# Performance work log

Measured on AMD Instinct MI355X. Metric: run time of the kernel, lower is better.

## Reference

```python
import jax, jax.numpy as jnp
import numpy as np

E = 16          # num_local_experts
K = 4           # experts_per_token
H = 2048        # hidden_size
I = 2048        # intermediate_size
LIMIT = 7.0     # swiglu_limit
ALPHA = 1.702   # glu_alpha


def setup_inputs() -> dict:
    key = jax.random.key(0)
    ks = jax.random.split(key, 9)
    int8 = lambda k, shp: jax.random.randint(k, shp, -127, 128).astype(jnp.float32)
    return {
        "hidden_states": jax.random.normal(ks[0], (1024, H), dtype=jnp.float32),
        "router_logits": jax.random.normal(ks[1], (1024, E), dtype=jnp.float32),
        "gate_up_proj": int8(ks[2], (E, H, 2 * I)),                      # int8 values in f32
        "gate_up_proj_scale": jax.random.uniform(ks[3], (E, 2 * I), minval=0.5, maxval=1.5) * 0.002,
        "gate_up_proj_bias": jax.random.normal(ks[4], (E, 2 * I), dtype=jnp.float32) * 0.01,
        "gate_up_smooth_scale": jnp.ones((E, I), dtype=jnp.float32),
        "down_proj": int8(ks[5], (E, I, H)),
        "down_proj_scale": jax.random.uniform(ks[6], (E, H), minval=0.5, maxval=1.5) * 0.002,
        "down_proj_bias": jax.random.normal(ks[7], (E, H), dtype=jnp.float32) * 0.01,
    }


def _dyn_quant(x):
    # per-token symmetric int8 dynamic quant (npu_dynamic_quant)
    scale = jnp.maximum(jnp.max(jnp.abs(x), axis=-1, keepdims=True) / 127.0, 1e-8)
    q = jnp.clip(jnp.round(x / scale), -127.0, 127.0)
    return q, scale


def reference(hidden_states, router_logits, gate_up_proj, gate_up_proj_scale,
              gate_up_proj_bias, gate_up_smooth_scale, down_proj,
              down_proj_scale, down_proj_bias):
    T = hidden_states.shape[0]
    C = (2 * T * K) // E

    # --- gating (npu_moe_gating_top_k: softmax + top-k, then renormalize) ---
    probs = jax.nn.softmax(router_logits, axis=-1)
    topk_w, topk_i = jax.lax.top_k(probs, K)                 # [T,K]
    topk_w = topk_w / jnp.sum(topk_w, axis=-1, keepdims=True)

    # --- per-token dynamic quant ---
    x_q, x_scale = _dyn_quant(hidden_states)                 # [T,H], [T,1]

    # --- dispatch (npu_moe_init_routing_v2): token-major expansion, capacity buckets ---
    flat_e = topk_i.reshape(-1)                              # [T*K] expert id per row
    flat_w = topk_w.reshape(-1)                              # [T*K]
    src = jnp.arange(T * K) // K                             # [T*K] source token
    onehot = jax.nn.one_hot(flat_e, E, dtype=jnp.int32)      # [T*K,E]
    pos = jnp.sum(jnp.cumsum(onehot, axis=0) * onehot, axis=1) - 1  # position within expert
    valid = pos < C
    slot = flat_e * C + jnp.where(valid, pos, 0)             # unique for valid rows
    vf = valid.astype(x_q.dtype)[:, None]
    x_disp = jnp.zeros((E * C, H), x_q.dtype).at[slot].add(x_q[src] * vf)
    s_disp = jnp.zeros((E * C, 1), x_scale.dtype).at[slot].add(x_scale[src] * vf)
    x_disp = x_disp.reshape(E, C, H)
    s_disp = s_disp.reshape(E, C, 1)

    gu_i32 = jnp.einsum('ech,ehf->ecf', x_disp, gate_up_proj)          # [E,C,2I]
    y = gu_i32 * s_disp * gate_up_proj_scale[:, None, :] + gate_up_proj_bias[:, None, :]

    # --- gpt-oss swiglu (activate_left, clamp_limit, alpha=1.702, glu_bias=1.0) ---
    gate = jnp.minimum(y[..., :I], LIMIT)
    up = jnp.clip(y[..., I:], -LIMIT, LIMIT)
    act = gate * jax.nn.sigmoid(ALPHA * gate) * (up + 1.0)
    act = act * gate_up_smooth_scale[:, None, :]

    # --- requant + grouped GEMM 2 + dequant ---
    h_q, h_scale = _dyn_quant(act)                                     # [E,C,I], [E,C,1]
    z_i32 = jnp.einsum('eci,eih->ech', h_q, down_proj)                 # [E,C,H]
    z = z_i32 * h_scale * down_proj_scale[:, None, :] + down_proj_bias[:, None, :]

    # --- combine (npu_moe_finalize_routing): weighted scatter-add per source token ---
    gathered = z.reshape(E * C, H)[slot]                               # [T*K,H]
    out = jnp.zeros((T, H), z.dtype).at[src].add(flat_w[:, None] * vf * gathered)
    return out
```

## Files before the change

### kernel.cpp

```cpp
#include <hip/hip_runtime.h>
#include <stdint.h>
#include <stddef.h>

#define T_TOK 1024
#define NE    16
#define TOPK  4
#define HID   2048
#define INTER 2048
#define CAP   512
#define GLIMIT 7.0f
#define GALPHA 1.702f

#define BM  128
#define BK  64

typedef __attribute__((ext_vector_type(4))) int   iv4;

typedef const __attribute__((address_space(1))) unsigned gl_u32;
typedef __attribute__((address_space(3))) unsigned lds_u32;
__device__ __forceinline__ void gl_lds16(const void* g, void* l) {
    __builtin_amdgcn_global_load_lds((gl_u32*)g, (lds_u32*)l, 16, 0, 0);
}

__device__ __forceinline__ int pack4(float a, float b, float c, float d) {
    int qa = (int)a, qb = (int)b, qc = (int)c, qd = (int)d;
    return (qa & 255) | ((qb & 255) << 8) | ((qc & 255) << 16) | (qd << 24);
}

__global__ __launch_bounds__(256) void gating_kernel(
    const float* __restrict__ logits, int* __restrict__ topki, float* __restrict__ topkw)
{
    int t = blockIdx.x * 256 + threadIdx.x;
    if (t >= T_TOK) return;
    float l[NE];
#pragma unroll
    for (int e = 0; e < NE; e++) l[e] = logits[t * NE + e];
    unsigned used = 0;
    float val[TOPK]; int idx[TOPK];
#pragma unroll
    for (int k = 0; k < TOPK; k++) {
        float bv = -3.4e38f; int bi = 0;
#pragma unroll
        for (int e = 0; e < NE; e++) {
            bool ok = (((used >> e) & 1u) == 0u) && (l[e] > bv);
            bv = ok ? l[e] : bv;
            bi = ok ? e : bi;
        }
        used |= (1u << bi); idx[k] = bi; val[k] = bv;
    }
    float m = val[0];
    float s = 0.f, w[TOPK];
#pragma unroll
    for (int k = 0; k < TOPK; k++) { w[k] = expf(val[k] - m); s += w[k]; }
    float inv = 1.0f / s;
#pragma unroll
    for (int k = 0; k < TOPK; k++) { topki[t * TOPK + k] = idx[k]; topkw[t * TOPK + k] = w[k] * inv; }
}

__global__ __launch_bounds__(256) void quant_x_kernel(
    const float* __restrict__ x, char* __restrict__ xq, float* __restrict__ xs)
{
    int t = blockIdx.x;
    const float4* row = (const float4*)(x + (size_t)t * HID);
    __shared__ float red[256];
    float4 v0 = row[threadIdx.x];
    float4 v1 = row[threadIdx.x + 256];
    float amax = fmaxf(fmaxf(fabsf(v0.x), fabsf(v0.y)), fmaxf(fabsf(v0.z), fabsf(v0.w)));
    amax = fmaxf(amax, fmaxf(fmaxf(fabsf(v1.x), fabsf(v1.y)), fmaxf(fabsf(v1.z), fabsf(v1.w))));
    red[threadIdx.x] = amax; __syncthreads();
    for (int s = 128; s > 0; s >>= 1) {
        if (threadIdx.x < s) red[threadIdx.x] = fmaxf(red[threadIdx.x], red[threadIdx.x + s]);
        __syncthreads();
    }
    float scale = fmaxf(red[0] / 127.0f, 1e-8f);
    if (threadIdx.x == 0) xs[t] = scale;
    char4* orow = (char4*)(xq + (size_t)t * HID);
    {
        char4 c;
        c.x = (char)fminf(fmaxf(rintf(v0.x / scale), -127.f), 127.f);
        c.y = (char)fminf(fmaxf(rintf(v0.y / scale), -127.f), 127.f);
        c.z = (char)fminf(fmaxf(rintf(v0.z / scale), -127.f), 127.f);
        c.w = (char)fminf(fmaxf(rintf(v0.w / scale), -127.f), 127.f);
        orow[threadIdx.x] = c;
        c.x = (char)fminf(fmaxf(rintf(v1.x / scale), -127.f), 127.f);
        c.y = (char)fminf(fmaxf(rintf(v1.y / scale), -127.f), 127.f);
        c.z = (char)fminf(fmaxf(rintf(v1.z / scale), -127.f), 127.f);
        c.w = (char)fminf(fmaxf(rintf(v1.w / scale), -127.f), 127.f);
        orow[threadIdx.x + 256] = c;
    }
}

__global__ __launch_bounds__(1024) void routing_kernel(
    const int* __restrict__ topki, const float* __restrict__ topkw,
    int* __restrict__ row_src, float* __restrict__ row_w, int* __restrict__ counts)
{
    int wv = threadIdx.x >> 6;
    int lane = threadIdx.x & 63;
    int base = 0;
    for (int r0 = 0; r0 < T_TOK * TOPK; r0 += 64) {
        int r = r0 + lane;
        int e = topki[r];
        unsigned long long mask = __ballot(e == wv);
        int pre = __popcll(mask & ((1ULL << lane) - 1ULL));
        if (e == wv) {
            int pos = base + pre;
            if (pos < CAP) {
                row_src[wv * CAP + pos] = r >> 2;
                row_w[wv * CAP + pos] = topkw[r];
            }
        }
        base += __popcll(mask);
    }
    if (lane == 0) counts[wv] = (base < CAP) ? base : CAP;
}

__global__ __launch_bounds__(256) void gemm1_kernel(
    const char* __restrict__ xq, const float* __restrict__ xs,
    const int* __restrict__ row_src, const int* __restrict__ counts,
    const float* __restrict__ gup, const float* __restrict__ gus,
    const float* __restrict__ gub, const float* __restrict__ smo,
    float* __restrict__ act)
{
    int nt = blockIdx.x;
    int mt = blockIdx.y;
    int e  = blockIdx.z;
    int count = counts[e];
    int m0 = mt * BM;
    if (m0 >= count) return;

    __shared__ char sA[BM * BK];
    __shared__ char sB[128 * BK];

    int t = threadIdx.x;
    int lane = t & 63, w = t >> 6;
    int n16 = lane & 15, quad = lane >> 4;
    int swq = quad ^ ((n16 >> 1) & 3);

    const char* aSrc[2];
#pragma unroll
    for (int op = 0; op < 2; op++) {
        int c = op * 256 + t;
        int row = c >> 2, ks = c & 3;
        int ksg = ks ^ ((row >> 1) & 3);
        int gr = m0 + row;
        if (gr > count - 1) gr = count - 1;
        aSrc[op] = xq + (size_t)row_src[e * CAP + gr] * HID + ksg * 16;
    }

    int bc = t & 63;
    const float* bgate = gup + (size_t)e * HID * (2 * INTER) + nt * 64 + bc;
    const float* bup   = bgate + INTER;
    int sn = (bc >> 1) & 3;
    char* wpg = sB + bc * 64        + (w ^ sn) * 16;
    char* wpu = sB + (64 + bc) * 64 + (w ^ sn) * 16;

    iv4 acc[2][8];
#pragma unroll
    for (int i = 0; i < 2; i++)
#pragma unroll
        for (int j = 0; j < 8; j++) acc[i][j] = (iv4)0;

    float f[32];
#pragma unroll
    for (int i = 0; i < 16; i++) {
        f[i]      = bgate[(size_t)(w * 16 + i) * (2 * INTER)];
        f[16 + i] = bup  [(size_t)(w * 16 + i) * (2 * INTER)];
    }

    for (int kt = 0; kt < HID / BK; kt++) {
        __syncthreads();
        gl_lds16(aSrc[0] + kt * BK, sA + w * 1024);
        gl_lds16(aSrc[1] + kt * BK, sA + 4096 + w * 1024);
        {
            int d0[4], d1[4];
#pragma unroll
            for (int j = 0; j < 4; j++) {
                d0[j] = pack4(f[4 * j],      f[4 * j + 1],      f[4 * j + 2],      f[4 * j + 3]);
                d1[j] = pack4(f[16 + 4 * j], f[16 + 4 * j + 1], f[16 + 4 * j + 2], f[16 + 4 * j + 3]);
            }
            *(int4*)wpg = make_int4(d0[0], d0[1], d0[2], d0[3]);
            *(int4*)wpu = make_int4(d1[0], d1[1], d1[2], d1[3]);
        }
        __syncthreads();

        iv4 af[2], bf[8];
#pragma unroll
        for (int mf = 0; mf < 2; mf++)
            af[mf] = *(const iv4*)(sA + (w * 32 + mf * 16 + n16) * 64 + swq * 16);
#pragma unroll
        for (int nf = 0; nf < 8; nf++)
            bf[nf] = *(const iv4*)(sB + (nf * 16 + n16) * 64 + swq * 16);

        int kn = (kt + 1 < HID / BK) ? (kt + 1) : kt;
        size_t krow = (size_t)(kn * BK) * (2 * INTER);
#pragma unroll
        for (int i = 0; i < 16; i++) {
            f[i]      = bgate[krow + (size_t)(w * 16 + i) * (2 * INTER)];
            f[16 + i] = bup  [krow + (size_t)(w * 16 + i) * (2 * INTER)];
        }

#pragma unroll
        for (int mf = 0; mf < 2; mf++)
#pragma unroll
            for (int nf = 0; nf < 8; nf++)
                acc[mf][nf] = __builtin_amdgcn_mfma_i32_16x16x64_i8(af[mf], bf[nf], acc[mf][nf], 0, 0, 0);
    }

    const float* gsc = gus + (size_t)e * (2 * INTER);
    const float* gbi = gub + (size_t)e * (2 * INTER);
    const float* sms = smo + (size_t)e * INTER;
#pragma unroll
    for (int mf = 0; mf < 2; mf++) {
#pragma unroll
        for (int r = 0; r < 4; r++) {
            int gr = m0 + w * 32 + mf * 16 + quad * 4 + r;
            if (gr >= count) continue;
            float srow = xs[row_src[e * CAP + gr]];
            float* arow = act + (size_t)(e * CAP + gr) * INTER;
#pragma unroll
            for (int g = 0; g < 4; g++) {
                int col = nt * 64 + g * 16 + n16;
                float yg = (float)acc[mf][g][r]     * srow * gsc[col]         + gbi[col];
                float yu = (float)acc[mf][g + 4][r] * srow * gsc[INTER + col] + gbi[INTER + col];
                float gate = fminf(yg, GLIMIT);
                float up   = fminf(fmaxf(yu, -GLIMIT), GLIMIT);
                float sig  = 1.0f / (1.0f + expf(-GALPHA * gate));
                arow[col] = gate * sig * (up + 1.0f) * sms[col];
            }
        }
    }
}

__global__ __launch_bounds__(256) void requant_kernel(
    const float* __restrict__ act, const int* __restrict__ counts,
    char* __restrict__ hq, float* __restrict__ hs)
{
    int b = blockIdx.x;
    int e = b >> 9, c = b & (CAP - 1);
    if (c >= counts[e]) return;
    const float4* row = (const float4*)(act + (size_t)b * INTER);
    __shared__ float red[256];
    float4 v0 = row[threadIdx.x];
    float4 v1 = row[threadIdx.x + 256];
    float amax = fmaxf(fmaxf(fabsf(v0.x), fabsf(v0.y)), fmaxf(fabsf(v0.z), fabsf(v0.w)));
    amax = fmaxf(amax, fmaxf(fmaxf(fabsf(v1.x), fabsf(v1.y)), fmaxf(fabsf(v1.z), fabsf(v1.w))));
    red[threadIdx.x] = amax; __syncthreads();
    for (int s = 128; s > 0; s >>= 1) {
        if (threadIdx.x < s) red[threadIdx.x] = fmaxf(red[threadIdx.x], red[threadIdx.x + s]);
        __syncthreads();
    }
    float scale = fmaxf(red[0] / 127.0f, 1e-8f);
    if (threadIdx.x == 0) hs[b] = scale;
    char4* orow = (char4*)(hq + (size_t)b * INTER);
    {
        char4 cc;
        cc.x = (char)fminf(fmaxf(rintf(v0.x / scale), -127.f), 127.f);
        cc.y = (char)fminf(fmaxf(rintf(v0.y / scale), -127.f), 127.f);
        cc.z = (char)fminf(fmaxf(rintf(v0.z / scale), -127.f), 127.f);
        cc.w = (char)fminf(fmaxf(rintf(v0.w / scale), -127.f), 127.f);
        orow[threadIdx.x] = cc;
        cc.x = (char)fminf(fmaxf(rintf(v1.x / scale), -127.f), 127.f);
        cc.y = (char)fminf(fmaxf(rintf(v1.y / scale), -127.f), 127.f);
        cc.z = (char)fminf(fmaxf(rintf(v1.z / scale), -127.f), 127.f);
        cc.w = (char)fminf(fmaxf(rintf(v1.w / scale), -127.f), 127.f);
        orow[threadIdx.x + 256] = cc;
    }
}

__global__ __launch_bounds__(256) void gemm2_kernel(
    const char* __restrict__ hq, const float* __restrict__ hs,
    const int* __restrict__ row_src, const float* __restrict__ row_w,
    const int* __restrict__ counts, const float* __restrict__ dwn,
    const float* __restrict__ dsc, const float* __restrict__ dbi,
    float* __restrict__ out)
{
    int nt = blockIdx.x;
    int mt = blockIdx.y;
    int e  = blockIdx.z;
    int count = counts[e];
    int m0 = mt * BM;
    if (m0 >= count) return;

    __shared__ char sA[BM * BK];
    __shared__ char sB[128 * BK];

    int t = threadIdx.x;
    int lane = t & 63, w = t >> 6;
    int n16 = lane & 15, quad = lane >> 4;
    int swq = quad ^ ((n16 >> 1) & 3);

    const char* aSrc[2];
#pragma unroll
    for (int op = 0; op < 2; op++) {
        int c = op * 256 + t;
        int row = c >> 2, ks = c & 3;
        int ksg = ks ^ ((row >> 1) & 3);
        int gr = m0 + row;
        if (gr > count - 1) gr = count - 1;
        aSrc[op] = hq + (size_t)(e * CAP + gr) * INTER + ksg * 16;
    }

    int bc = t & 127;
    int half = t >> 7;
    const float* bsrc = dwn + (size_t)e * INTER * HID + nt * 128 + bc;
    int sn = (bc >> 1) & 3;
    char* wp0 = sB + bc * 64 + ((half * 2 + 0) ^ sn) * 16;
    char* wp1 = sB + bc * 64 + ((half * 2 + 1) ^ sn) * 16;

    iv4 acc[2][8];
#pragma unroll
    for (int i = 0; i < 2; i++)
#pragma unroll
        for (int j = 0; j < 8; j++) acc[i][j] = (iv4)0;

    float f[32];
#pragma unroll
    for (int i = 0; i < 32; i++)
        f[i] = bsrc[(size_t)(half * 32 + i) * HID];

    for (int kt = 0; kt < INTER / BK; kt++) {
        __syncthreads();
        gl_lds16(aSrc[0] + kt * BK, sA + w * 1024);
        gl_lds16(aSrc[1] + kt * BK, sA + 4096 + w * 1024);
        {
            int d[8];
#pragma unroll
            for (int j = 0; j < 8; j++)
                d[j] = pack4(f[4 * j], f[4 * j + 1], f[4 * j + 2], f[4 * j + 3]);
            *(int4*)wp0 = make_int4(d[0], d[1], d[2], d[3]);
            *(int4*)wp1 = make_int4(d[4], d[5], d[6], d[7]);
        }
        __syncthreads();

        iv4 af[2], bf[8];
#pragma unroll
        for (int mf = 0; mf < 2; mf++)
            af[mf] = *(const iv4*)(sA + (w * 32 + mf * 16 + n16) * 64 + swq * 16);
#pragma unroll
        for (int nf = 0; nf < 8; nf++)
            bf[nf] = *(const iv4*)(sB + (nf * 16 + n16) * 64 + swq * 16);

        int kn = (kt + 1 < INTER / BK) ? (kt + 1) : kt;
        size_t krow = (size_t)(kn * BK) * HID;
#pragma unroll
        for (int i = 0; i < 32; i++)
            f[i] = bsrc[krow + (size_t)(half * 32 + i) * HID];

#pragma unroll
        for (int mf = 0; mf < 2; mf++)
#pragma unroll
            for (int nf = 0; nf < 8; nf++)
                acc[mf][nf] = __builtin_amdgcn_mfma_i32_16x16x64_i8(af[mf], bf[nf], acc[mf][nf], 0, 0, 0);
    }

    const float* dscE = dsc + (size_t)e * HID;
    const float* dbiE = dbi + (size_t)e * HID;
#pragma unroll
    for (int mf = 0; mf < 2; mf++) {
#pragma unroll
        for (int r = 0; r < 4; r++) {
            int gr = m0 + w * 32 + mf * 16 + quad * 4 + r;
            if (gr >= count) continue;
            int ri = e * CAP + gr;
            float hsr = hs[ri];
            float wr  = row_w[ri];
            float* orow = out + (size_t)row_src[ri] * HID;
#pragma unroll
            for (int nf = 0; nf < 8; nf++) {
                int col = nt * 128 + nf * 16 + n16;
                float z = (float)acc[mf][nf][r] * hsr * dscE[col] + dbiE[col];
                atomicAdd(&orow[col], wr * z);
            }
        }
    }
}

extern "C" void kernel_launch(void* const* d_in, const int* in_sizes, int n_in,
                              void* d_out, int out_size, void* d_ws, size_t ws_size,
                              hipStream_t stream)
{
    (void)in_sizes; (void)n_in; (void)out_size; (void)ws_size;
    const float* x   = (const float*)d_in[0];
    const float* rl  = (const float*)d_in[1];
    const float* gup = (const float*)d_in[2];
    const float* gus = (const float*)d_in[3];
    const float* gub = (const float*)d_in[4];
    const float* smo = (const float*)d_in[5];
    const float* dwn = (const float*)d_in[6];
    const float* dsc = (const float*)d_in[7];
    const float* dbi = (const float*)d_in[8];
    float* out = (float*)d_out;

    char* p = (char*)d_ws;
    auto carve = [&](size_t bytes) -> char* {
        char* r = p; p += (bytes + 255) & ~(size_t)255; return r;
    };
    char* xq       = carve((size_t)T_TOK * HID);
    float* xs      = (float*)carve((size_t)T_TOK * 4);
    int* topki     = (int*)carve((size_t)T_TOK * TOPK * 4);
    float* topkw   = (float*)carve((size_t)T_TOK * TOPK * 4);
    int* counts    = (int*)carve((size_t)NE * 4);
    int* rsrc      = (int*)carve((size_t)NE * CAP * 4);
    float* rw      = (float*)carve((size_t)NE * CAP * 4);
    float* actb    = (float*)carve((size_t)NE * CAP * INTER * 4);
    char* hq       = carve((size_t)NE * CAP * INTER);
    float* hsb     = (float*)carve((size_t)NE * CAP * 4);

    hipMemsetAsync(d_out, 0, (size_t)T_TOK * HID * 4, stream);
    gating_kernel<<<dim3((T_TOK + 255) / 256), 256, 0, stream>>>(rl, topki, topkw);
    quant_x_kernel<<<dim3(T_TOK), 256, 0, stream>>>(x, xq, xs);
    routing_kernel<<<dim3(1), 1024, 0, stream>>>(topki, topkw, rsrc, rw, counts);
    gemm1_kernel<<<dim3(INTER / 64, CAP / BM, NE), 256, 0, stream>>>(
        xq, xs, rsrc, counts, gup, gus, gub, smo, actb);
    requant_kernel<<<dim3(NE * CAP), 256, 0, stream>>>(actb, counts, hq, hsb);
    gemm2_kernel<<<dim3(HID / 128, CAP / BM, NE), 256, 0, stream>>>(
        hq, hsb, rsrc, rw, counts, dwn, dsc, dbi, out);
}
```

Measured before the change: 1.066 ms.

## Double-buffer LDS tiles in both grouped GEMM kernels

Both grouped GEMM kernels now use two LDS buffers for the A and B tiles. The next k-tile's async A loads and B register loads are issued before the current tile's MFMAs, and the packed B is written into the alternate buffer afterwards. This cuts the loop from two barriers per k-step to one and lets global loads overlap compute. In exchange, shared memory per block doubles to 32 KB, which may reduce occupancy.

```diff
diff --git a/kernel.cpp b/kernel.cpp
--- a/kernel.cpp
+++ b/kernel.cpp
@@ -128,8 +128,8 @@
     int m0 = mt * BM;
     if (m0 >= count) return;
 
-    __shared__ char sA[BM * BK];
-    __shared__ char sB[128 * BK];
+    __shared__ char sA[2 * BM * BK];
+    __shared__ char sB[2 * 128 * BK];
 
     int t = threadIdx.x;
     int lane = t & 63, w = t >> 6;
@@ -151,8 +151,8 @@
     const float* bgate = gup + (size_t)e * HID * (2 * INTER) + nt * 64 + bc;
     const float* bup   = bgate + INTER;
     int sn = (bc >> 1) & 3;
-    char* wpg = sB + bc * 64        + (w ^ sn) * 16;
-    char* wpu = sB + (64 + bc) * 64 + (w ^ sn) * 16;
+    int wpgOff = bc * 64        + (w ^ sn) * 16;
+    int wpuOff = (64 + bc) * 64 + (w ^ sn) * 16;
 
     iv4 acc[2][8];
 #pragma unroll
@@ -160,50 +160,63 @@
 #pragma unroll
         for (int j = 0; j < 8; j++) acc[i][j] = (iv4)0;
 
+    const int NT = HID / BK;
     float f[32];
+    gl_lds16(aSrc[0], sA + w * 1024);
+    gl_lds16(aSrc[1], sA + 4096 + w * 1024);
 #pragma unroll
     for (int i = 0; i < 16; i++) {
         f[i]      = bgate[(size_t)(w * 16 + i) * (2 * INTER)];
         f[16 + i] = bup  [(size_t)(w * 16 + i) * (2 * INTER)];
     }
-
-    for (int kt = 0; kt < HID / BK; kt++) {
-        __syncthreads();
-        gl_lds16(aSrc[0] + kt * BK, sA + w * 1024);
-        gl_lds16(aSrc[1] + kt * BK, sA + 4096 + w * 1024);
-        {
+    {
+        int d0[4], d1[4];
+#pragma unroll
+        for (int j = 0; j < 4; j++) {
+            d0[j] = pack4(f[4 * j],      f[4 * j + 1],      f[4 * j + 2],      f[4 * j + 3]);
+            d1[j] = pack4(f[16 + 4 * j], f[16 + 4 * j + 1], f[16 + 4 * j + 2], f[16 + 4 * j + 3]);
+        }
+        *(int4*)(sB + wpgOff) = make_int4(d0[0], d0[1], d0[2], d0[3]);
+        *(int4*)(sB + wpuOff) = make_int4(d1[0], d1[1], d1[2], d1[3]);
+    }
+    __syncthreads();
+
+    for (int kt = 0; kt < NT; kt++) {
+        int p = kt & 1;
+        bool more = (kt + 1) < NT;
+        if (more) {
+            gl_lds16(aSrc[0] + (kt + 1) * BK, sA + (p ^ 1) * 8192 + w * 1024);
+            gl_lds16(aSrc[1] + (kt + 1) * BK, sA + (p ^ 1) * 8192 + 4096 + w * 1024);
+            size_t krow = (size_t)((kt + 1) * BK) * (2 * INTER);
+#pragma unroll
+            for (int i = 0; i < 16; i++) {
+                f[i]      = bgate[krow + (size_t)(w * 16 + i) * (2 * INTER)];
+                f[16 + i] = bup  [krow + (size_t)(w * 16 + i) * (2 * INTER)];
+            }
+        }
+        iv4 af[2], bf[8];
+#pragma unroll
+        for (int mf = 0; mf < 2; mf++)
+            af[mf] = *(const iv4*)(sA + p * 8192 + (w * 32 + mf * 16 + n16) * 64 + swq * 16);
+#pragma unroll
+        for (int nf = 0; nf < 8; nf++)
+            bf[nf] = *(const iv4*)(sB + p * 8192 + (nf * 16 + n16) * 64 + swq * 16);
+#pragma unroll
+        for (int mf = 0; mf < 2; mf++)
+#pragma unroll
+            for (int nf = 0; nf < 8; nf++)
+                acc[mf][nf] = __builtin_amdgcn_mfma_i32_16x16x64_i8(af[mf], bf[nf], acc[mf][nf], 0, 0, 0);
+        if (more) {
             int d0[4], d1[4];
 #pragma unroll
             for (int j = 0; j < 4; j++) {
                 d0[j] = pack4(f[4 * j],      f[4 * j + 1],      f[4 * j + 2],      f[4 * j + 3]);
                 d1[j] = pack4(f[16 + 4 * j], f[16 + 4 * j + 1], f[16 + 4 * j + 2], f[16 + 4 * j + 3]);
             }
-            *(int4*)wpg = make_int4(d0[0], d0[1], d0[2], d0[3]);
-            *(int4*)wpu = make_int4(d1[0], d1[1], d1[2], d1[3]);
-        }
-        __syncthreads();
-
-        iv4 af[2], bf[8];
-#pragma unroll
-        for (int mf = 0; mf < 2; mf++)
-            af[mf] = *(const iv4*)(sA + (w * 32 + mf * 16 + n16) * 64 + swq * 16);
-#pragma unroll
-        for (int nf = 0; nf < 8; nf++)
-            bf[nf] = *(const iv4*)(sB + (nf * 16 + n16) * 64 + swq * 16);
-
-        int kn = (kt + 1 < HID / BK) ? (kt + 1) : kt;
-        size_t krow = (size_t)(kn * BK) * (2 * INTER);
-#pragma unroll
-        for (int i = 0; i < 16; i++) {
-            f[i]      = bgate[krow + (size_t)(w * 16 + i) * (2 * INTER)];
-            f[16 + i] = bup  [krow + (size_t)(w * 16 + i) * (2 * INTER)];
-        }
-
-#pragma unroll
-        for (int mf = 0; mf < 2; mf++)
-#pragma unroll
-            for (int nf = 0; nf < 8; nf++)
-                acc[mf][nf] = __builtin_amdgcn_mfma_i32_16x16x64_i8(af[mf], bf[nf], acc[mf][nf], 0, 0, 0);
+            *(int4*)(sB + (p ^ 1) * 8192 + wpgOff) = make_int4(d0[0], d0[1], d0[2], d0[3]);
+            *(int4*)(sB + (p ^ 1) * 8192 + wpuOff) = make_int4(d1[0], d1[1], d1[2], d1[3]);
+            __syncthreads();
+        }
     }
 
     const float* gsc = gus + (size_t)e * (2 * INTER);
@@ -281,8 +294,8 @@
     int m0 = mt * BM;
     if (m0 >= count) return;
 
-    __shared__ char sA[BM * BK];
-    __shared__ char sB[128 * BK];
+    __shared__ char sA[2 * BM * BK];
+    __shared__ char sB[2 * 128 * BK];
 
     int t = threadIdx.x;
     int lane = t & 63, w = t >> 6;
@@ -304,8 +317,8 @@
     int half = t >> 7;
     const float* bsrc = dwn + (size_t)e * INTER * HID + nt * 128 + bc;
     int sn = (bc >> 1) & 3;
-    char* wp0 = sB + bc * 64 + ((half * 2 + 0) ^ sn) * 16;
-    char* wp1 = sB + bc * 64 + ((half * 2 + 1) ^ sn) * 16;
+    int wp0Off = bc * 64 + ((half * 2 + 0) ^ sn) * 16;
+    int wp1Off = bc * 64 + ((half * 2 + 1) ^ sn) * 16;
 
     iv4 acc[2][8];
 #pragma unroll
@@ -313,44 +326,55 @@
 #pragma unroll
         for (int j = 0; j < 8; j++) acc[i][j] = (iv4)0;
 
+    const int NT = INTER / BK;
     float f[32];
+    gl_lds16(aSrc[0], sA + w * 1024);
+    gl_lds16(aSrc[1], sA + 4096 + w * 1024);
 #pragma unroll
     for (int i = 0; i < 32; i++)
         f[i] = bsrc[(size_t)(half * 32 + i) * HID];
-
-    for (int kt = 0; kt < INTER / BK; kt++) {
-        __syncthreads();
-        gl_lds16(aSrc[0] + kt * BK, sA + w * 1024);
-        gl_lds16(aSrc[1] + kt * BK, sA + 4096 + w * 1024);
-        {
+    {
+        int d[8];
+#pragma unroll
+        for (int j = 0; j < 8; j++)
+            d[j] = pack4(f[4 * j], f[4 * j + 1], f[4 * j + 2], f[4 * j + 3]);
+        *(int4*)(sB + wp0Off) = make_int4(d[0], d[1], d[2], d[3]);
+        *(int4*)(sB + wp1Off) = make_int4(d[4], d[5], d[6], d[7]);
+    }
+    __syncthreads();
+
+    for (int kt = 0; kt < NT; kt++) {
+        int p = kt & 1;
+        bool more = (kt + 1) < NT;
+        if (more) {
+            gl_lds16(aSrc[0] + (kt + 1) * BK, sA + (p ^ 1) * 8192 + w * 1024);
+            gl_lds16(aSrc[1] + (kt + 1) * BK, sA + (p ^ 1) * 8192 + 4096 + w * 1024);
+            size_t krow = (size_t)((kt + 1) * BK) * HID;
+#pragma unroll
+            for (int i = 0; i < 32; i++)
+                f[i] = bsrc[krow + (size_t)(half * 32 + i) * HID];
+        }
+        iv4 af[2], bf[8];
+#pragma unroll
+        for (int mf = 0; mf < 2; mf++)
+            af[mf] = *(const iv4*)(sA + p * 8192 + (w * 32 + mf * 16 + n16) * 64 + swq * 16);
+#pragma unroll
+        for (int nf = 0; nf < 8; nf++)
+            bf[nf] = *(const iv4*)(sB + p * 8192 + (nf * 16 + n16) * 64 + swq * 16);
+#pragma unroll
+        for (int mf = 0; mf < 2; mf++)
+#pragma unroll
+            for (int nf = 0; nf < 8; nf++)
+                acc[mf][nf] = __builtin_amdgcn_mfma_i32_16x16x64_i8(af[mf], bf[nf], acc[mf][nf], 0, 0, 0);
+        if (more) {
             int d[8];
 #pragma unroll
             for (int j = 0; j < 8; j++)
                 d[j] = pack4(f[4 * j], f[4 * j + 1], f[4 * j + 2], f[4 * j + 3]);
-            *(int4*)wp0 = make_int4(d[0], d[1], d[2], d[3]);
-            *(int4*)wp1 = make_int4(d[4], d[5], d[6], d[7]);
-        }
-        __syncthreads();
-
-        iv4 af[2], bf[8];
-#pragma unroll
-        for (int mf = 0; mf < 2; mf++)
-            af[mf] = *(const iv4*)(sA + (w * 32 + mf * 16 + n16) * 64 + swq * 16);
-#pragma unroll
-        for (int nf = 0; nf < 8; nf++)
-            bf[nf] = *(const iv4*)(sB + (nf * 16 + n16) * 64 + swq * 16);
-
-        int kn = (kt + 1 < INTER / BK) ? (kt + 1) : kt;
-        size_t krow = (size_t)(kn * BK) * HID;
-#pragma unroll
-        for (int i = 0; i < 32; i++)
-            f[i] = bsrc[krow + (size_t)(half * 32 + i) * HID];
-
-#pragma unroll
-        for (int mf = 0; mf < 2; mf++)
-#pragma unroll
-            for (int nf = 0; nf < 8; nf++)
-                acc[mf][nf] = __builtin_amdgcn_mfma_i32_16x16x64_i8(af[mf], bf[nf], acc[mf][nf], 0, 0, 0);
+            *(int4*)(sB + (p ^ 1) * 8192 + wp0Off) = make_int4(d[0], d[1], d[2], d[3]);
+            *(int4*)(sB + (p ^ 1) * 8192 + wp1Off) = make_int4(d[4], d[5], d[6], d[7]);
+            __syncthreads();
+        }
     }
 
     const float* dscE = dsc + (size_t)e * HID;
```

New measurement: 1.136 ms. 6.6% more time.
